# Kernel tuning notes

Hardware: AMD Instinct MI355X
Metric: run time of the kernel (lower is better)

Reference implementation:

```python
import jax, jax.numpy as jnp
import numpy as np
from jax import lax

LAM = 0.1
NUM_ITERS = 20
SIGNAL_LENGTH = 4096


def _conv1d_same(x, k):
    # x: [B, L], k: [K]. TF tf.nn.conv1d is cross-correlation with SAME padding
    # (pad_total = K-1, lo = (K-1)//2), which matches lax 'SAME'.
    return lax.conv_general_dilated(x[:, None, :], k[None, None, :],
                                    window_strides=(1,), padding='SAME')[:, 0, :]


def setup_inputs() -> dict:
    key = jax.random.key(0)
    ks = jax.random.split(key, 4)
    B, L, K, H = 4096, SIGNAL_LENGTH, 64, 256
    y = jax.random.normal(ks[0], (B, L), jnp.float32)
    thz_pulse = jax.random.normal(ks[1], (K,), jnp.float32)
    W1 = jax.random.normal(ks[2], (L, H), jnp.float32) * 0.02
    b1 = jnp.zeros((H,), jnp.float32)
    W2 = jax.random.normal(ks[3], (H, 1), jnp.float32) * 0.02
    b2 = jnp.zeros((1,), jnp.float32)
    return {"y": y, "thz_pulse": thz_pulse, "W1": W1, "b1": b1, "W2": W2, "b2": b2}


def reference(y, thz_pulse, W1, b1, W2, b2):
    # tf.reverse of the pulse + TF cross-correlation == convolution with the pulse
    kernel = thz_pulse[::-1]
    # L (Lipschitz const) was a non-trainable Variable: no gradient through it
    L_const = lax.stop_gradient(jnp.sum(thz_pulse * thz_pulse))
    theta = LAM / L_const
    B_term = _conv1d_same(y, kernel) / L_const  # [B, L], constant across iterations

    def step(x, _):
        c = B_term + x - _conv1d_same(x, kernel) / L_const
        x_new = jnp.sign(c) * jnp.maximum(jnp.abs(c) - theta, 0.0)  # soft-threshold
        return x_new, None

    x, _ = lax.scan(step, jnp.zeros_like(y), None, length=NUM_ITERS)

    features = jax.nn.relu(x @ W1 + b1)          # [B, 256]
    peak_pred = (features @ W2 + b2)[:, 0] * SIGNAL_LENGTH  # [B]
    return x, peak_pred
```

## Files before the change

### kernel.cpp

```cpp
#include <hip/hip_runtime.h>

typedef __attribute__((ext_vector_type(4))) float f32x4;
typedef __attribute__((ext_vector_type(8))) short short8;
typedef __attribute__((ext_vector_type(4))) short short4v;

#define PADW(I) ((I) + ((I) >> 4))
#define WOFF(z) ((z) + ((z) >> 4))

constexpr int LROW = 4096;
constexpr int KW   = 64;
constexpr int HALO = 32;
constexpr int NLOG = LROW + 2 * HALO;
constexpr int XS_SIZE = PADW(NLOG - 1) + 1;

constexpr int AS    = 8384;
constexpr int SLOT  = 3 * AS;
constexpr int POOLB = 2 * SLOT;
static_assert(XS_SIZE * 4 <= SLOT, "y f32 stage fits in buf1 region");

__device__ __forceinline__ float bfh2f(unsigned short h) {
  return __uint_as_float(((unsigned)h) << 16);
}
__device__ __forceinline__ unsigned short btrunc(float x) {
  return (unsigned short)(__float_as_uint(x) >> 16);
}
__device__ __forceinline__ void split3s(float x, unsigned short& h,
                                        unsigned short& m, unsigned short& l) {
  h = btrunc(x);
  float r1 = (x - bfh2f(h)) * 256.0f;
  m = btrunc(r1);
  float r2 = (r1 - bfh2f(m)) * 256.0f;
  l = btrunc(r2);
}
__device__ __forceinline__ float shrinkf(float c, float theta) {
  float a = fabsf(c) - theta;
  return (a > 0.0f) ? copysignf(a, c) : 0.0f;
}

__device__ __forceinline__ void conv_row(const float* __restrict__ xw,
                                         const float* __restrict__ kn,
                                         float acc[16]) {
#pragma unroll
  for (int e = 0; e < 16; ++e) acc[e] = 0.0f;
#pragma unroll
  for (int m = 0; m < 79; ++m) {
    float wv = xw[WOFF(1 + m)];
    const int jlo = (m - 15 > 0) ? (m - 15) : 0;
    const int jhi = (m < 63) ? m : 63;
#pragma unroll
    for (int j = jlo; j <= jhi; ++j) acc[m - j] = fmaf(kn[j], wv, acc[m - j]);
  }
}

__global__ __launch_bounds__(256, 3) void ista_mfma(
    const float* __restrict__ y, const float* __restrict__ pulse,
    float* __restrict__ xout) {
  __shared__ __align__(16) char pool[POOLB];
  __shared__ float pl[KW];
  __shared__ float knl[KW];

  const int t = threadIdx.x, w = t >> 6, l = t & 63, lc = l & 15, kb = l >> 4;
  const int row = blockIdx.x;

  if (t < KW) pl[t] = pulse[t];

#pragma unroll
  for (int a = 0; a < 3; ++a) {
    char* ab = pool + a * AS;
    if (t < 16) *(unsigned*)(ab + 4 * t) = 0u;
    if (t < 24) *(unsigned*)(ab + 8256 + 4 * t) = 0u;
  }

  float* yw = (float*)(pool + SLOT);
  if (t < HALO) { yw[PADW(t)] = 0.0f; yw[PADW(NLOG - HALO + t)] = 0.0f; }
  const float* yrow = y + (size_t)row * LROW;
#pragma unroll
  for (int q = 0; q < 4; ++q) {
    int i4 = q * 256 + t; float4 v = ((const float4*)yrow)[i4];
    yw[PADW(HALO + 4 * i4 + 0)] = v.x; yw[PADW(HALO + 4 * i4 + 1)] = v.y;
    yw[PADW(HALO + 4 * i4 + 2)] = v.z; yw[PADW(HALO + 4 * i4 + 3)] = v.w;
  }
  __syncthreads();

  float Lc = 0.0f;
#pragma unroll
  for (int j = 0; j < KW; ++j) Lc += pl[j] * pl[j];
  const float theta = 0.1f / Lc, invL = 1.0f / Lc;
  if (t < KW) knl[t] = pl[KW - 1 - t] / Lc;

  short8 Ah[3], Am[3], Al[3];
#pragma unroll
  for (int kf = 0; kf < 3; ++kf) {
#pragma unroll
    for (int j = 0; j < 8; ++j) {
      int q = 32 * kf + 8 * kb + j, d = q - lc - 1;
      float v = (d >= 0 && d < 64) ? pl[63 - d] * invL : 0.0f;
      float vc = ((q == lc + 32) ? 1.0f : 0.0f) - v;
      unsigned short h, m, lo; split3s(vc, h, m, lo);
      Ah[kf][j] = (short)h; Am[kf][j] = (short)m; Al[kf][j] = (short)lo;
    }
  }
  __syncthreads();

  float bts[16];
  conv_row(yw + 17 * t, knl, bts);
  __syncthreads();

#pragma unroll
  for (int e = 0; e < 16; ++e) (yw + 17 * t)[WOFF(32 + e)] = bts[e];
  __syncthreads();

  f32x4 bt[4];
#pragma unroll
  for (int T = 0; T < 4; ++T) {
    const int n0 = 1024 * w + 256 * T + 16 * lc + 4 * kb;
#pragma unroll
    for (int i = 0; i < 4; ++i) bt[T][i] = yw[PADW(HALO + n0 + i)];
  }
  __syncthreads();

#pragma unroll
  for (int a = 0; a < 3; ++a) {
    char* ab = pool + SLOT + a * AS;
    if (t < 16) *(unsigned*)(ab + 4 * t) = 0u;
    if (t < 24) *(unsigned*)(ab + 8256 + 4 * t) = 0u;
  }
  const int rb_lane = 2048 * w + 32 * lc + 16 * kb;
  const int wb_lane = 2048 * w + 32 * lc + 8 * kb + 64;
  {
    char* wp = pool + SLOT + wb_lane;
#pragma unroll
    for (int T = 0; T < 4; ++T) {
      short4v h4, m4, l4;
#pragma unroll
      for (int i = 0; i < 4; ++i) {
        float xn = shrinkf(bt[T][i], theta);
        unsigned short h, m, lo; split3s(xn, h, m, lo);
        h4[i] = (short)h; m4[i] = (short)m; l4[i] = (short)lo;
      }
      *(short4v*)(wp + 512 * T)          = h4;
      *(short4v*)(wp + 512 * T + AS)     = m4;
      *(short4v*)(wp + 512 * T + 2 * AS) = l4;
    }
  }
  __syncthreads();

  constexpr float S8 = 1.0f / 256.0f, S16 = 1.0f / 65536.0f;

  for (int it = 0; it < 19; ++it) {
    const int rs = (it & 1) ? 0 : SLOT, ws = (it & 1) ? SLOT : 0;
    const char* rp = pool + rs + rb_lane;
    char* wp = pool + ws + wb_lane;
#pragma unroll
    for (int T = 0; T < 4; ++T) {
      f32x4 ah = bt[T], am = (f32x4)0.0f, al = (f32x4)0.0f;
#pragma unroll
      for (int kf = 0; kf < 3; ++kf) {
        const char* p = rp + 512 * T + 64 * kf;
        short8 xh = *(const short8*)(p);
        short8 xm = *(const short8*)(p + AS);
        short8 xl = *(const short8*)(p + 2 * AS);
        ah = __builtin_amdgcn_mfma_f32_16x16x32_bf16(Ah[kf], xh, ah, 0, 0, 0);
        am = __builtin_amdgcn_mfma_f32_16x16x32_bf16(Ah[kf], xm, am, 0, 0, 0);
        am = __builtin_amdgcn_mfma_f32_16x16x32_bf16(Am[kf], xh, am, 0, 0, 0);
        al = __builtin_amdgcn_mfma_f32_16x16x32_bf16(Ah[kf], xl, al, 0, 0, 0);
        al = __builtin_amdgcn_mfma_f32_16x16x32_bf16(Am[kf], xm, al, 0, 0, 0);
        al = __builtin_amdgcn_mfma_f32_16x16x32_bf16(Al[kf], xh, al, 0, 0, 0);
      }
      short4v h4, m4, l4;
#pragma unroll
      for (int i = 0; i < 4; ++i) {
        float c  = fmaf(S16, al[i], fmaf(S8, am[i], ah[i]));
        float xn = shrinkf(c, theta);
        unsigned short h, m, lo; split3s(xn, h, m, lo);
        h4[i] = (short)h; m4[i] = (short)m; l4[i] = (short)lo;
      }
      *(short4v*)(wp + 512 * T)          = h4;
      *(short4v*)(wp + 512 * T + AS)     = m4;
      *(short4v*)(wp + 512 * T + 2 * AS) = l4;
    }
    __syncthreads();
  }

  {
    const char* hp = pool + 64 + 32 * t;
    float o[16];
#pragma unroll
    for (int s = 0; s < 2; ++s) {
      short8 hv = *(const short8*)(hp + 16 * s);
      short8 mv = *(const short8*)(hp + AS + 16 * s);
      short8 lv = *(const short8*)(hp + 2 * AS + 16 * s);
#pragma unroll
      for (int c2 = 0; c2 < 8; ++c2) {
        float xv = fmaf(S8, bfh2f((unsigned short)mv[c2]),
                        bfh2f((unsigned short)hv[c2]));
        o[8 * s + c2] = fmaf(S16, bfh2f((unsigned short)lv[c2]), xv);
      }
    }
    float4* xr = (float4*)(xout + (size_t)row * LROW + 16 * t);
#pragma unroll
    for (int s = 0; s < 4; ++s)
      xr[s] = make_float4(o[4 * s], o[4 * s + 1], o[4 * s + 2], o[4 * s + 3]);
  }
}

__device__ __forceinline__ unsigned short f2bf(float f) {
  unsigned u = __float_as_uint(f);
  u += 0x7fffu + ((u >> 16) & 1u);
  return (unsigned short)(u >> 16);
}

__global__ __launch_bounds__(256) void cast_w1(const float* __restrict__ W1,
                                               unsigned short* __restrict__ W1p) {
  const int kq = blockIdx.x;
  const int c  = threadIdx.x;
  short8 v;
#pragma unroll
  for (int j = 0; j < 8; ++j)
    v[j] = (short)f2bf(W1[(size_t)(kq * 8 + j) * 256 + c]);
  *(short8*)(W1p + ((size_t)kq * 256 + c) * 8) = v;
}

__global__ __launch_bounds__(256) void mlp_mfma(
    const float* __restrict__ x, const unsigned short* __restrict__ W1p,
    const float* __restrict__ b1, const float* __restrict__ W2,
    const float* __restrict__ b2, float* __restrict__ out1) {
  __shared__ short Ap[16 * 8 * 8];
  __shared__ short Bp[8 * 256 * 8];
  __shared__ float pr[4][16];

  const int t = threadIdx.x;
  const int w = t >> 6;
  const int l = t & 63;
  const int lrow = l & 15;
  const int lk   = l >> 4;
  const int row0 = blockIdx.x * 16;

  f32x4 acc[4];
#pragma unroll
  for (int n = 0; n < 4; ++n) acc[n] = (f32x4)0.0f;

  for (int kt = 0; kt < 64; ++kt) {
    __syncthreads();
    {
      const int r  = t >> 4;
      const int k4 = t & 15;
      const float4 v = *(const float4*)(x + (size_t)(row0 + r) * LROW + kt * 64 + k4 * 4);
      short4v a;
      a.x = (short)f2bf(v.x); a.y = (short)f2bf(v.y);
      a.z = (short)f2bf(v.z); a.w = (short)f2bf(v.w);
      const int kq = k4 >> 1, h = k4 & 1;
      *(short4v*)((char*)Ap + ((r * 8 + (kq ^ (r & 7))) * 16 + h * 8)) = a;
    }
    {
      const short8* src = (const short8*)(W1p + (size_t)kt * (8 * 256 * 8));
      short8* dst = (short8*)Bp;
#pragma unroll
      for (int i = 0; i < 8; ++i) dst[t + 256 * i] = src[t + 256 * i];
    }
    __syncthreads();
#pragma unroll
    for (int kf = 0; kf < 2; ++kf) {
      const int kq = kf * 4 + lk;
      short8 af = *(short8*)((char*)Ap + (lrow * 8 + (kq ^ (lrow & 7))) * 16);
#pragma unroll
      for (int n = 0; n < 4; ++n) {
        short8 bf = *(short8*)((char*)Bp + (kq * 256 + w * 64 + n * 16 + lrow) * 16);
        acc[n] = __builtin_amdgcn_mfma_f32_16x16x32_bf16(af, bf, acc[n], 0, 0, 0);
      }
    }
  }

  float s[4] = {0.0f, 0.0f, 0.0f, 0.0f};
#pragma unroll
  for (int n = 0; n < 4; ++n) {
    const int c = w * 64 + n * 16 + lrow;
    const float b1v = b1[c];
    const float w2v = W2[c];
#pragma unroll
    for (int i = 0; i < 4; ++i) {
      float f = acc[n][i] + b1v;
      f = fmaxf(f, 0.0f);
      s[i] = fmaf(f, w2v, s[i]);
    }
  }
#pragma unroll
  for (int off = 1; off < 16; off <<= 1) {
#pragma unroll
    for (int i = 0; i < 4; ++i) s[i] += __shfl_xor(s[i], off, 64);
  }
  if (lrow == 0) {
#pragma unroll
    for (int i = 0; i < 4; ++i) pr[w][lk * 4 + i] = s[i];
  }
  __syncthreads();
  if (t < 16) {
    out1[row0 + t] =
        (pr[0][t] + pr[1][t] + pr[2][t] + pr[3][t] + b2[0]) * (float)LROW;
  }
}

extern "C" void kernel_launch(void* const* d_in, const int* in_sizes, int n_in,
                              void* d_out, int out_size, void* d_ws, size_t ws_size,
                              hipStream_t stream) {
  const float* y     = (const float*)d_in[0];
  const float* pulse = (const float*)d_in[1];
  const float* W1    = (const float*)d_in[2];
  const float* b1    = (const float*)d_in[3];
  const float* W2    = (const float*)d_in[4];
  const float* b2    = (const float*)d_in[5];

  float* xout = (float*)d_out;
  float* out1 = xout + (size_t)LROW * LROW;
  unsigned short* W1p = (unsigned short*)d_ws;

  cast_w1<<<512, 256, 0, stream>>>(W1, W1p);
  ista_mfma<<<LROW, 256, 0, stream>>>(y, pulse, xout);
  mlp_mfma<<<LROW / 16, 256, 0, stream>>>(xout, W1p, b1, W2, b2, out1);
}
```

Before: 399.6 us.

## Switch ISTA Toeplitz MFMA to 32x32x16 tiles with padded LDS layout

```diff
diff --git a/kernel.cpp b/kernel.cpp
--- a/kernel.cpp
+++ b/kernel.cpp
@@ -1,6 +1,7 @@
 #include <hip/hip_runtime.h>
 
 typedef __attribute__((ext_vector_type(4))) float f32x4;
+typedef __attribute__((ext_vector_type(16))) float f32x16;
 typedef __attribute__((ext_vector_type(8))) short short8;
 typedef __attribute__((ext_vector_type(4))) short short4v;
 
@@ -13,10 +14,11 @@
 constexpr int NLOG = LROW + 2 * HALO;
 constexpr int XS_SIZE = PADW(NLOG - 1) + 1;
 
-constexpr int AS    = 8384;
+constexpr int AS    = 10384;
 constexpr int SLOT  = 3 * AS;
 constexpr int POOLB = 2 * SLOT;
-static_assert(XS_SIZE * 4 <= SLOT, "y f32 stage fits in buf1 region");
+static_assert(XS_SIZE * 4 <= SLOT, "f32 y stage fits in buf1 region");
+static_assert(POOLB + 2 * KW * 4 <= 65536, "static LDS limit");
 
 __device__ __forceinline__ float bfh2f(unsigned short h) {
   return __uint_as_float(((unsigned)h) << 16);
@@ -52,14 +54,16 @@
   }
 }
 
-__global__ __launch_bounds__(256, 3) void ista_mfma(
+__global__ __launch_bounds__(256, 2) void ista_mfma(
     const float* __restrict__ y, const float* __restrict__ pulse,
     float* __restrict__ xout) {
   __shared__ __align__(16) char pool[POOLB];
   __shared__ float pl[KW];
   __shared__ float knl[KW];
 
-  const int t = threadIdx.x, w = t >> 6, l = t & 63, lc = l & 15, kb = l >> 4;
+  const int t = threadIdx.x, w = t >> 6, l = t & 63;
+  const int lq = l & 31;
+  const int hi = l >> 5;
   const int row = blockIdx.x;
 
   if (t < KW) pl[t] = pulse[t];
@@ -68,7 +72,7 @@
   for (int a = 0; a < 3; ++a) {
     char* ab = pool + a * AS;
     if (t < 16) *(unsigned*)(ab + 4 * t) = 0u;
-    if (t < 24) *(unsigned*)(ab + 8256 + 4 * t) = 0u;
+    if (t < 16) *(unsigned*)(ab + 10320 + 4 * t) = 0u;
   }
 
   float* yw = (float*)(pool + SLOT);
@@ -86,16 +90,16 @@
 #pragma unroll
   for (int j = 0; j < KW; ++j) Lc += pl[j] * pl[j];
   const float theta = 0.1f / Lc, invL = 1.0f / Lc;
-  if (t < KW) knl[t] = pl[KW - 1 - t] / Lc;
-
-  short8 Ah[3], Am[3], Al[3];
-#pragma unroll
-  for (int kf = 0; kf < 3; ++kf) {
+  if (t < KW) knl[t] = pl[KW - 1 - t] * invL;
+
+  short8 Ah[6], Am[6], Al[6];
+#pragma unroll
+  for (int kf = 0; kf < 6; ++kf) {
 #pragma unroll
     for (int j = 0; j < 8; ++j) {
-      int q = 32 * kf + 8 * kb + j, d = q - lc - 1;
+      int q = 16 * kf + 8 * hi + j, d = q - lq - 1;
       float v = (d >= 0 && d < 64) ? pl[63 - d] * invL : 0.0f;
-      float vc = ((q == lc + 32) ? 1.0f : 0.0f) - v;
+      float vc = ((q == lq + 32) ? 1.0f : 0.0f) - v;
       unsigned short h, m, lo; split3s(vc, h, m, lo);
       Ah[kf][j] = (short)h; Am[kf][j] = (short)m; Al[kf][j] = (short)lo;
     }
@@ -110,12 +114,11 @@
   for (int e = 0; e < 16; ++e) (yw + 17 * t)[WOFF(32 + e)] = bts[e];
   __syncthreads();
 
-  f32x4 bt[4];
-#pragma unroll
-  for (int T = 0; T < 4; ++T) {
-    const int n0 = 1024 * w + 256 * T + 16 * lc + 4 * kb;
-#pragma unroll
-    for (int i = 0; i < 4; ++i) bt[T][i] = yw[PADW(HALO + n0 + i)];
+  f32x16 bt;
+#pragma unroll
+  for (int r = 0; r < 16; ++r) {
+    const int e = (r & 3) + 8 * (r >> 2) + 4 * hi;
+    bt[r] = yw[PADW(32 + 1024 * w + 32 * lq + e)];
   }
   __syncthreads();
 
@@ -123,73 +126,87 @@
   for (int a = 0; a < 3; ++a) {
     char* ab = pool + SLOT + a * AS;
     if (t < 16) *(unsigned*)(ab + 4 * t) = 0u;
-    if (t < 24) *(unsigned*)(ab + 8256 + 4 * t) = 0u;
-  }
-  const int rb_lane = 2048 * w + 32 * lc + 16 * kb;
-  const int wb_lane = 2048 * w + 32 * lc + 8 * kb + 64;
+    if (t < 16) *(unsigned*)(ab + 10320 + 4 * t) = 0u;
+  }
+
+  const int rbL = 80 * (32 * w + lq) + 16 * hi;
+  const int wbL = 80 * (32 * w + lq + 1) + 8 * hi;
+  constexpr float S8 = 1.0f / 256.0f, S16 = 1.0f / 65536.0f;
+
   {
-    char* wp = pool + SLOT + wb_lane;
-#pragma unroll
-    for (int T = 0; T < 4; ++T) {
+    unsigned short hh[16], mm[16], ll[16];
+#pragma unroll
+    for (int i = 0; i < 16; ++i) {
+      float xn = shrinkf(bt[i], theta);
+      split3s(xn, hh[i], mm[i], ll[i]);
+    }
+    char* wpb = pool + SLOT;
+#pragma unroll
+    for (int g = 0; g < 4; ++g) {
       short4v h4, m4, l4;
 #pragma unroll
       for (int i = 0; i < 4; ++i) {
-        float xn = shrinkf(bt[T][i], theta);
-        unsigned short h, m, lo; split3s(xn, h, m, lo);
-        h4[i] = (short)h; m4[i] = (short)m; l4[i] = (short)lo;
+        h4[i] = (short)hh[4 * g + i]; m4[i] = (short)mm[4 * g + i];
+        l4[i] = (short)ll[4 * g + i];
       }
-      *(short4v*)(wp + 512 * T)          = h4;
-      *(short4v*)(wp + 512 * T + AS)     = m4;
-      *(short4v*)(wp + 512 * T + 2 * AS) = l4;
-    }
-  }
-  __syncthreads();
-
-  constexpr float S8 = 1.0f / 256.0f, S16 = 1.0f / 65536.0f;
+      char* wp = wpb + wbL + 16 * g;
+      *(short4v*)(wp)          = h4;
+      *(short4v*)(wp + AS)     = m4;
+      *(short4v*)(wp + 2 * AS) = l4;
+    }
+  }
+  __syncthreads();
 
   for (int it = 0; it < 19; ++it) {
-    const int rs = (it & 1) ? 0 : SLOT, ws = (it & 1) ? SLOT : 0;
-    const char* rp = pool + rs + rb_lane;
-    char* wp = pool + ws + wb_lane;
-#pragma unroll
-    for (int T = 0; T < 4; ++T) {
-      f32x4 ah = bt[T], am = (f32x4)0.0f, al = (f32x4)0.0f;
-#pragma unroll
-      for (int kf = 0; kf < 3; ++kf) {
-        const char* p = rp + 512 * T + 64 * kf;
-        short8 xh = *(const short8*)(p);
-        short8 xm = *(const short8*)(p + AS);
-        short8 xl = *(const short8*)(p + 2 * AS);
-        ah = __builtin_amdgcn_mfma_f32_16x16x32_bf16(Ah[kf], xh, ah, 0, 0, 0);
-        am = __builtin_amdgcn_mfma_f32_16x16x32_bf16(Ah[kf], xm, am, 0, 0, 0);
-        am = __builtin_amdgcn_mfma_f32_16x16x32_bf16(Am[kf], xh, am, 0, 0, 0);
-        al = __builtin_amdgcn_mfma_f32_16x16x32_bf16(Ah[kf], xl, al, 0, 0, 0);
-        al = __builtin_amdgcn_mfma_f32_16x16x32_bf16(Am[kf], xm, al, 0, 0, 0);
-        al = __builtin_amdgcn_mfma_f32_16x16x32_bf16(Al[kf], xh, al, 0, 0, 0);
+    const int rs = (it & 1) ? 0 : SLOT, ws = SLOT - rs;
+    const char* rp = pool + rs + rbL;
+    f32x16 ah = bt, am = (f32x16)0.0f, al = (f32x16)0.0f;
+#pragma unroll
+    for (int kf = 0; kf < 6; ++kf) {
+      const char* p = rp + (32 * kf + 16 * (kf >> 1));
+      short8 xh = *(const short8*)(p);
+      short8 xm = *(const short8*)(p + AS);
+      short8 xl = *(const short8*)(p + 2 * AS);
+      ah = __builtin_amdgcn_mfma_f32_32x32x16_bf16(Ah[kf], xh, ah, 0, 0, 0);
+      am = __builtin_amdgcn_mfma_f32_32x32x16_bf16(Ah[kf], xm, am, 0, 0, 0);
+      am = __builtin_amdgcn_mfma_f32_32x32x16_bf16(Am[kf], xh, am, 0, 0, 0);
+      al = __builtin_amdgcn_mfma_f32_32x32x16_bf16(Ah[kf], xl, al, 0, 0, 0);
+      al = __builtin_amdgcn_mfma_f32_32x32x16_bf16(Am[kf], xm, al, 0, 0, 0);
+      al = __builtin_amdgcn_mfma_f32_32x32x16_bf16(Al[kf], xh, al, 0, 0, 0);
+    }
+    unsigned short hh[16], mm[16], ll[16];
+#pragma unroll
+    for (int i = 0; i < 16; ++i) {
+      float c  = fmaf(S16, al[i], fmaf(S8, am[i], ah[i]));
+      float xn = shrinkf(c, theta);
+      split3s(xn, hh[i], mm[i], ll[i]);
+    }
+    char* wpb = pool + ws;
+#pragma unroll
+    for (int g = 0; g < 4; ++g) {
+      short4v h4, m4, l4;
+#pragma unroll
+      for (int i = 0; i < 4; ++i) {
+        h4[i] = (short)hh[4 * g + i]; m4[i] = (short)mm[4 * g + i];
+        l4[i] = (short)ll[4 * g + i];
       }
-      short4v h4, m4, l4;
-#pragma unroll
-      for (int i = 0; i < 4; ++i) {
-        float c  = fmaf(S16, al[i], fmaf(S8, am[i], ah[i]));
-        float xn = shrinkf(c, theta);
-        unsigned short h, m, lo; split3s(xn, h, m, lo);
-        h4[i] = (short)h; m4[i] = (short)m; l4[i] = (short)lo;
-      }
-      *(short4v*)(wp + 512 * T)          = h4;
-      *(short4v*)(wp + 512 * T + AS)     = m4;
-      *(short4v*)(wp + 512 * T + 2 * AS) = l4;
+      char* wp = wpb + wbL + 16 * g;
+      *(short4v*)(wp)          = h4;
+      *(short4v*)(wp + AS)     = m4;
+      *(short4v*)(wp + 2 * AS) = l4;
     }
     __syncthreads();
   }
 
   {
-    const char* hp = pool + 64 + 32 * t;
+    const int base = 32 * t + 64 + 16 * ((t + 2) >> 1);
     float o[16];
 #pragma unroll
     for (int s = 0; s < 2; ++s) {
-      short8 hv = *(const short8*)(hp + 16 * s);
-      short8 mv = *(const short8*)(hp + AS + 16 * s);
-      short8 lv = *(const short8*)(hp + 2 * AS + 16 * s);
+      const char* hp = pool + base + 16 * s;
+      short8 hv = *(const short8*)(hp);
+      short8 mv = *(const short8*)(hp + AS);
+      short8 lv = *(const short8*)(hp + 2 * AS);
 #pragma unroll
       for (int c2 = 0; c2 < 8; ++c2) {
         float xv = fmaf(S8, bfh2f((unsigned short)mv[c2]),
```

Result: slower. 420.5 us (+5.2%).
